# Performance work log

Hardware: AMD Instinct MI355X
Metric: run time of the kernel (lower is better)

The kernel has to match this reference:

```python
import jax, jax.numpy as jnp
import numpy as np

ALPHA = 0.2  # LeakyReLU negative slope
EPS = 1e-8


def setup_inputs() -> dict:
    key = jax.random.key(0)
    ks = jax.random.split(key, 7)
    N, Fin, Fout, E = 100000, 256, 128, 800000
    node_embedding = jax.random.normal(ks[0], (N, Fin), dtype=jnp.float32)
    adj_pos = jax.random.randint(ks[1], (2, E), 0, N, dtype=jnp.int64)
    adj_neg = jax.random.randint(ks[2], (2, E), 0, N, dtype=jnp.int64)
    edge_embedding = jax.random.normal(ks[3], (2, Fout), dtype=jnp.float32)
    Wr = jax.random.normal(ks[4], (2, Fin, Fout), dtype=jnp.float32) * 0.05
    a = jax.random.normal(ks[5], (1, 2 * Fout), dtype=jnp.float32) * 0.05
    bias = jax.random.normal(ks[6], (1, Fout), dtype=jnp.float32) * 0.05
    return dict(node_embedding=node_embedding, edge_embedding=edge_embedding,
                Wr=Wr, a=a, bias=bias, adj_pos=adj_pos, adj_neg=adj_neg)


def reference(node_embedding, edge_embedding, Wr, a, bias, adj_pos, adj_neg):
    N = node_embedding.shape[0]
    Fout = Wr.shape[2]
    # h_r = X @ Wr[r], then column-scale by edge_embedding[r] (== mm with diag)
    h_pos = (node_embedding @ Wr[0]) * edge_embedding[0]  # [N, Fout]
    h_neg = (node_embedding @ Wr[1]) * edge_embedding[1]  # [N, Fout]
    a_src = a[0, :Fout]  # attention weights for source half of concat
    a_dst = a[0, Fout:]  # attention weights for dest half

    def edge_scores(h, adj):
        # a . [h[src], h[dst]] computed as node-level dots then scalar gather
        s = h @ a_src  # [N]
        d = h @ a_dst  # [N]
        z = s[adj[0]] + d[adj[1]]  # [E]
        z = jnp.where(z > 0, z, ALPHA * z)  # LeakyReLU
        return jax.nn.sigmoid(z)

    e_pos = edge_scores(h_pos, adj_pos)  # [E_pos]
    e_neg = edge_scores(h_neg, adj_neg)  # [E_neg]

    # row-sum normalizer: spmm(edge, edge_e, ones) == segment_sum over row idx
    rows = jnp.concatenate([adj_pos[0], adj_neg[0]])
    e_all = jnp.concatenate([e_pos, e_neg])
    row_sum = jax.ops.segment_sum(e_all, rows, num_segments=N) + EPS  # [N]

    # weighted aggregation: out[i] = sum_{(i,j)} e_ij * h[j]
    agg = (jax.ops.segment_sum(e_pos[:, None] * h_pos[adj_pos[1]], adj_pos[0], num_segments=N)
           + jax.ops.segment_sum(e_neg[:, None] * h_neg[adj_neg[1]], adj_neg[0], num_segments=N))
    return agg / row_sum[:, None] + bias
```

## Files before the change

kernel.cpp:

```cpp
#include <hip/hip_runtime.h>

#define ALPHA 0.2f
#define EPSV 1e-8f
#define BUCK_BITS 8
#define BUCK (1 << BUCK_BITS)
#define CAP 5120
#define EPB_A 4096
#define EPT_A (EPB_A / 256)

typedef float f32x4 __attribute__((ext_vector_type(4)));
typedef short bf16x8 __attribute__((ext_vector_type(8)));

static __device__ __forceinline__ unsigned short f2bf(float f) {
    union { float f; unsigned int u; } c; c.f = f;
    unsigned int u = c.u;
    unsigned int round = ((u >> 16) & 1) + 0x7FFF;
    return (unsigned short)((u + round) >> 16);
}
static __device__ __forceinline__ float bflo(unsigned int u) {
    union { unsigned int u; float f; } c; c.u = u << 16; return c.f;
}
static __device__ __forceinline__ float bfhi(unsigned int u) {
    union { unsigned int u; float f; } c; c.u = u & 0xFFFF0000u; return c.f;
}

__global__ __launch_bounds__(256) void convB_binA_kernel(
    const float* __restrict__ Wr, uint4* __restrict__ Bp,
    const int* __restrict__ adj_pos, const int* __restrict__ adj_neg,
    int* __restrict__ bucketCount, unsigned int* __restrict__ edges_tmp,
    int N, int E)
{
    __shared__ int hist[512];
    __shared__ int base[512];
    __shared__ int cur[512];
    const int tid = threadIdx.x;

    if ((int)blockIdx.x < 32) {
        const int t = blockIdx.x * 256 + tid;
        const int kb  = t >> 8;
        const int col = t & 255;
        const int rel = col >> 7;
        const int cc  = col & 127;
        unsigned short v[8];
        #pragma unroll
        for (int jj = 0; jj < 8; ++jj) {
            const int k = kb * 8 + jj;
            v[jj] = f2bf(Wr[(size_t)rel * 256 * 128 + (size_t)k * 128 + cc]);
        }
        Bp[t] = *reinterpret_cast<const uint4*>(v);
        return;
    }

    const int bb = blockIdx.x - 32;
    const long long e0 = (long long)bb * EPB_A;
    const long long twoE = 2LL * E;

    hist[tid] = 0;
    hist[tid + 256] = 0;

    int esrc[EPT_A];
    unsigned int erec[EPT_A];
    #pragma unroll
    for (int k = 0; k < EPT_A; ++k) {
        const long long idx = e0 + (long long)k * 256 + tid;
        if (idx < twoE) {
            const int rel = (idx >= E) ? 1 : 0;
            const long long eidx = rel ? idx - E : idx;
            const int* __restrict__ adj = rel ? adj_neg : adj_pos;
            const int src = adj[eidx];
            const int dst = adj[E + eidx];
            esrc[k] = src;
            erec[k] = (unsigned int)dst | ((unsigned int)rel << 17) |
                      ((unsigned int)(src & (BUCK - 1)) << 18);
        } else {
            esrc[k] = -1;
        }
    }
    __syncthreads();

    #pragma unroll
    for (int k = 0; k < EPT_A; ++k)
        if (esrc[k] >= 0) atomicAdd(&hist[esrc[k] >> BUCK_BITS], 1);
    __syncthreads();

    {
        const int rot = (bb * 61) & 511;
        #pragma unroll
        for (int q = 0; q < 2; ++q) {
            const int t2 = (tid + q * 256 + rot) & 511;
            const int hv = hist[t2];
            base[t2] = hv ? atomicAdd(&bucketCount[t2], hv) : 0;
            cur[t2] = 0;
        }
    }
    __syncthreads();

    #pragma unroll
    for (int k = 0; k < EPT_A; ++k) {
        if (esrc[k] >= 0) {
            const int b = esrc[k] >> BUCK_BITS;
            const int r = atomicAdd(&cur[b], 1);
            const int pos = base[b] + r;
            if (pos < CAP)
                edges_tmp[(size_t)b * CAP + pos] = erec[k];
        }
    }
}

__global__ __launch_bounds__(256) void mfma_gemm_kernel(
    const float* __restrict__ X, const uint4* __restrict__ Bp,
    const float* __restrict__ ee, const float* __restrict__ a,
    unsigned short* __restrict__ h, float* __restrict__ sd, int N)
{
    __shared__ unsigned short Alds[32 * 256];
    const int tid  = threadIdx.x;
    const int lane = tid & 63;
    const int w    = tid >> 6;
    const int wm   = w >> 1;
    const int wn   = w & 1;
    const int cl   = lane & 15;
    const int g    = lane >> 4;
    const int tile0 = blockIdx.x * 32;

    #pragma unroll
    for (int pass = 0; pass < 4; ++pass) {
        const int L  = pass * 256 + tid;
        const int r  = L >> 5;
        const int c8 = L & 31;
        const int row = tile0 + r;
        float4 f0 = make_float4(0.f, 0.f, 0.f, 0.f);
        float4 f1 = make_float4(0.f, 0.f, 0.f, 0.f);
        if (row < N) {
            const float* xp = &X[(size_t)row * 256 + c8 * 8];
            f0 = *reinterpret_cast<const float4*>(xp);
            f1 = *reinterpret_cast<const float4*>(xp + 4);
        }
        unsigned short v[8];
        v[0]=f2bf(f0.x); v[1]=f2bf(f0.y); v[2]=f2bf(f0.z); v[3]=f2bf(f0.w);
        v[4]=f2bf(f1.x); v[5]=f2bf(f1.y); v[6]=f2bf(f1.z); v[7]=f2bf(f1.w);
        const int su = c8 ^ (r & 7);
        *reinterpret_cast<bf16x8*>(&Alds[r * 256 + su * 8]) =
            *reinterpret_cast<const bf16x8*>(v);
    }
    __syncthreads();

    f32x4 acc[8];
    #pragma unroll
    for (int ct = 0; ct < 8; ++ct)
        acc[ct] = (f32x4){0.f, 0.f, 0.f, 0.f};

    const int rl = wm * 16 + cl;
    #pragma unroll
    for (int kc = 0; kc < 8; ++kc) {
        const int ku = kc * 4 + g;
        const int su = ku ^ (rl & 7);
        const bf16x8 af = *reinterpret_cast<const bf16x8*>(&Alds[rl * 256 + su * 8]);
        bf16x8 bfr[8];
        #pragma unroll
        for (int ct = 0; ct < 8; ++ct) {
            const int col = wn * 128 + ct * 16 + cl;
            bfr[ct] = *reinterpret_cast<const bf16x8*>(Bp + ku * 256 + col);
        }
        #pragma unroll
        for (int ct = 0; ct < 8; ++ct)
            acc[ct] = __builtin_amdgcn_mfma_f32_16x16x32_bf16(
                af, bfr[ct], acc[ct], 0, 0, 0);
    }

    const int rt = blockIdx.x * 2 + wm;
    float eev[8], asv[8], adv[8];
    #pragma unroll
    for (int ct = 0; ct < 8; ++ct) {
        const int col = wn * 128 + ct * 16 + cl;
        const int cc  = col & 127;
        eev[ct] = ee[col];
        asv[ct] = a[cc];
        adv[ct] = a[128 + cc];
    }

    float s_acc[4], d_acc[4];
    #pragma unroll
    for (int reg = 0; reg < 4; ++reg) {
        const int row = rt * 16 + g * 4 + reg;
        const bool ok = row < N;
        float sp = 0.f, dp = 0.f;
        #pragma unroll
        for (int ct = 0; ct < 8; ++ct) {
            const float v = acc[ct][reg] * eev[ct];
            sp += v * asv[ct];
            dp += v * adv[ct];
            if (ok) {
                const int cc = ct * 16 + cl;
                h[((size_t)wn * N + row) * 128 + cc] = f2bf(v);
            }
        }
        s_acc[reg] = sp;
        d_acc[reg] = dp;
    }
    #pragma unroll
    for (int reg = 0; reg < 4; ++reg) {
        float sp = s_acc[reg], dp = d_acc[reg];
        #pragma unroll
        for (int off = 1; off < 16; off <<= 1) {
            sp += __shfl_xor(sp, off);
            dp += __shfl_xor(dp, off);
        }
        if (cl == 0) {
            const int row = rt * 16 + g * 4 + reg;
            if (row < N) {
                sd[(size_t)wn * 2 * N + row]     = sp;
                sd[(size_t)wn * 2 * N + N + row] = dp;
            }
        }
    }
}

__global__ __launch_bounds__(512) void sortB_kernel(
    const int* __restrict__ bucketCount, const unsigned int* __restrict__ edges_tmp,
    const float* __restrict__ sd,
    uint2* __restrict__ edges_final,
    int* __restrict__ rowBeg, int* __restrict__ rowEnd,
    float* __restrict__ rowSum, int N)
{
    __shared__ int hist[BUCK];
    __shared__ int cur[BUCK];
    __shared__ int ssum[BUCK];
    __shared__ float sSrc[2][BUCK];
    __shared__ float rsLds[BUCK];
    const int tid = threadIdx.x;
    const int b   = blockIdx.x;
    const int s0  = b << BUCK_BITS;
    const size_t tb = (size_t)b * CAP;
    const int cnt = min(bucketCount[b], CAP);

    if (tid < BUCK) {
        hist[tid] = 0;
        rsLds[tid] = 0.f;
        const int gsrc = s0 + tid;
        sSrc[0][tid] = (gsrc < N) ? sd[gsrc] : 0.f;
        sSrc[1][tid] = (gsrc < N) ? sd[2 * (size_t)N + gsrc] : 0.f;
    }
    __syncthreads();
    for (int j = tid; j < cnt; j += 512)
        atomicAdd(&hist[edges_tmp[tb + j] >> 18], 1);
    __syncthreads();

    int h0 = 0, incl = 0;
    if (tid < BUCK) { h0 = hist[tid]; ssum[tid] = h0; incl = h0; }
    __syncthreads();
    for (int off = 1; off < BUCK; off <<= 1) {
        const int u = (tid < BUCK && tid >= off) ? ssum[tid - off] : 0;
        __syncthreads();
        if (tid < BUCK) { incl += u; ssum[tid] = incl; }
        __syncthreads();
    }
    if (tid < BUCK) {
        const int excl = incl - h0;
        cur[tid] = excl;
        const int gidx = s0 + tid;
        if (gidx < N) {
            rowBeg[gidx] = (int)tb + excl;
            rowEnd[gidx] = (int)tb + incl;
        }
    }
    __syncthreads();
    for (int j = tid; j < cnt; j += 512) {
        const unsigned int r = edges_tmp[tb + j];
        const int sl  = r >> 18;
        const int rel = (r >> 17) & 1;
        const int dst = r & 0x1FFFF;
        float z = sSrc[rel][sl] + sd[(size_t)rel * 2 * N + N + dst];
        z = z > 0.f ? z : ALPHA * z;
        const float ev = 1.f / (1.f + __expf(-z));
        const int pos = atomicAdd(&cur[sl], 1);
        atomicAdd(&rsLds[sl], ev);
        edges_final[tb + pos] =
            make_uint2((unsigned int)(rel * N + dst), __float_as_uint(ev));
    }
    __syncthreads();
    if (tid < BUCK) {
        const int gidx = s0 + tid;
        if (gidx < N) rowSum[gidx] = rsLds[tid];
    }
}

__global__ __launch_bounds__(256) void gather_kernel(
    const int* __restrict__ rowBeg, const int* __restrict__ rowEnd,
    const float* __restrict__ rowSum,
    const uint2* __restrict__ edges,
    const unsigned short* __restrict__ h,
    const float* __restrict__ bias, float* __restrict__ out, int N)
{
    const long long gw = ((long long)blockIdx.x * blockDim.x + threadIdx.x) >> 6;
    const int lane = threadIdx.x & 63;
    if (gw >= N) return;
    const int n = (int)gw;

    const int beg = rowBeg[n];
    const int end = rowEnd[n];
    const unsigned loff = (unsigned)(lane << 2);
    const char* __restrict__ hb = (const char*)h;

    float ax = 0.f, ay = 0.f;
    int j = beg;
    for (; j + 8 <= end; j += 8) {
        uint2 r[8];
        #pragma unroll
        for (int k = 0; k < 8; ++k) r[k] = edges[j + k];
        unsigned int hv[8];
        #pragma unroll
        for (int k = 0; k < 8; ++k)
            hv[k] = *reinterpret_cast<const unsigned int*>(
                hb + ((r[k].x << 8) + loff));
        #pragma unroll
        for (int k = 0; k < 8; ++k) {
            const float e = __uint_as_float(r[k].y);
            ax += e * bflo(hv[k]);
            ay += e * bfhi(hv[k]);
        }
    }
    for (; j + 4 <= end; j += 4) {
        uint2 r[4];
        #pragma unroll
        for (int k = 0; k < 4; ++k) r[k] = edges[j + k];
        unsigned int hv[4];
        #pragma unroll
        for (int k = 0; k < 4; ++k)
            hv[k] = *reinterpret_cast<const unsigned int*>(
                hb + ((r[k].x << 8) + loff));
        #pragma unroll
        for (int k = 0; k < 4; ++k) {
            const float e = __uint_as_float(r[k].y);
            ax += e * bflo(hv[k]);
            ay += e * bfhi(hv[k]);
        }
    }
    for (; j < end; ++j) {
        const uint2 r = edges[j];
        const unsigned int hv = *reinterpret_cast<const unsigned int*>(
            hb + ((r.x << 8) + loff));
        const float e = __uint_as_float(r.y);
        ax += e * bflo(hv);
        ay += e * bfhi(hv);
    }
    const float inv = 1.f / (rowSum[n] + EPSV);
    const float2 bv = *reinterpret_cast<const float2*>(&bias[lane * 2]);
    float2 o;
    o.x = ax * inv + bv.x;
    o.y = ay * inv + bv.y;
    *reinterpret_cast<float2*>(&out[(size_t)n * 128 + lane * 2]) = o;
}

extern "C" void kernel_launch(void* const* d_in, const int* in_sizes, int n_in,
                              void* d_out, int out_size, void* d_ws, size_t ws_size,
                              hipStream_t stream) {
    const float* X      = (const float*)d_in[0];
    const float* ee     = (const float*)d_in[1];
    const float* Wr     = (const float*)d_in[2];
    const float* a      = (const float*)d_in[3];
    const float* bias   = (const float*)d_in[4];
    const int* adj_pos  = (const int*)d_in[5];
    const int* adj_neg  = (const int*)d_in[6];

    const int N = in_sizes[0] / 256;
    const int E = in_sizes[5] / 2;
    const int twoE = 2 * E;
    float* out = (float*)d_out;

    const int gemmBlocks = (N + 31) / 32;
    const int NBUCK = (N + BUCK - 1) >> BUCK_BITS;
    const int binBlocks = (twoE + EPB_A - 1) / EPB_A;

    char* ws = (char*)d_ws;
    uint4* Bp = (uint4*)ws;
    char* p = ws + 32 * 256 * 16;
    unsigned short* h = (unsigned short*)p; p += (size_t)2 * N * 128 * 2;
    float* sd         = (float*)p;  p += (size_t)4 * N * 4;
    int* bucketCount  = (int*)p;    p += 512 * 4;
    int* rowBeg       = (int*)p;    p += (size_t)N * 4;
    int* rowEnd       = (int*)p;    p += (size_t)N * 4;
    float* rowSum     = (float*)p;  p += (size_t)N * 4;
    p = (char*)(((uintptr_t)p + 15) & ~(uintptr_t)15);
    unsigned int* edges_tmp = (unsigned int*)p; p += (size_t)NBUCK * CAP * 4;
    uint2* edges_final = (uint2*)p; p += (size_t)NBUCK * CAP * 8;

    (void)hipMemsetAsync(bucketCount, 0, 512 * sizeof(int), stream);

    convB_binA_kernel<<<32 + binBlocks, 256, 0, stream>>>(
        Wr, Bp, adj_pos, adj_neg, bucketCount, edges_tmp, N, E);

    mfma_gemm_kernel<<<gemmBlocks, 256, 0, stream>>>(X, Bp, ee, a, h, sd, N);

    sortB_kernel<<<NBUCK, 512, 0, stream>>>(
        bucketCount, edges_tmp, sd, edges_final, rowBeg, rowEnd, rowSum, N);

    gather_kernel<<<(int)(((long long)N * 64 + 255) / 256), 256, 0, stream>>>(
        rowBeg, rowEnd, rowSum, edges_final, (const unsigned short*)h, bias, out, N);
}
```

Measured before the change: 169.7 us.

## Pack h as bf16 pairs, prefetch GEMM operands, batch X loads

The GEMM epilogue now packs two bf16 outputs into one 32-bit store using a permuted column layout, replacing eight 2-byte scattered stores per row. The gather kernel un-permutes the columns when writing the output. The GEMM also issues all X global loads before converting any of them, and double-buffers the B/A fragments across k-steps to overlap loads with MFMA. These changes raise register pressure, and the gather output stores become scalar rather than float2.

```diff
diff --git a/kernel.cpp b/kernel.cpp
--- a/kernel.cpp
+++ b/kernel.cpp
@@ -110,7 +110,7 @@
 __global__ __launch_bounds__(256) void mfma_gemm_kernel(
     const float* __restrict__ X, const uint4* __restrict__ Bp,
     const float* __restrict__ ee, const float* __restrict__ a,
-    unsigned short* __restrict__ h, float* __restrict__ sd, int N)
+    unsigned int* __restrict__ h32, float* __restrict__ sd, int N)
 {
     __shared__ unsigned short Alds[32 * 256];
     const int tid  = threadIdx.x;
@@ -122,25 +122,36 @@
     const int g    = lane >> 4;
     const int tile0 = blockIdx.x * 32;
 
-    #pragma unroll
-    for (int pass = 0; pass < 4; ++pass) {
-        const int L  = pass * 256 + tid;
-        const int r  = L >> 5;
-        const int c8 = L & 31;
-        const int row = tile0 + r;
-        float4 f0 = make_float4(0.f, 0.f, 0.f, 0.f);
-        float4 f1 = make_float4(0.f, 0.f, 0.f, 0.f);
-        if (row < N) {
-            const float* xp = &X[(size_t)row * 256 + c8 * 8];
-            f0 = *reinterpret_cast<const float4*>(xp);
-            f1 = *reinterpret_cast<const float4*>(xp + 4);
-        }
-        unsigned short v[8];
-        v[0]=f2bf(f0.x); v[1]=f2bf(f0.y); v[2]=f2bf(f0.z); v[3]=f2bf(f0.w);
-        v[4]=f2bf(f1.x); v[5]=f2bf(f1.y); v[6]=f2bf(f1.z); v[7]=f2bf(f1.w);
-        const int su = c8 ^ (r & 7);
-        *reinterpret_cast<bf16x8*>(&Alds[r * 256 + su * 8]) =
-            *reinterpret_cast<const bf16x8*>(v);
+    {
+        float4 fa[4], fb[4];
+        #pragma unroll
+        for (int pass = 0; pass < 4; ++pass) {
+            const int L  = pass * 256 + tid;
+            const int r  = L >> 5;
+            const int c8 = L & 31;
+            const int row = tile0 + r;
+            fa[pass] = make_float4(0.f, 0.f, 0.f, 0.f);
+            fb[pass] = make_float4(0.f, 0.f, 0.f, 0.f);
+            if (row < N) {
+                const float* xp = &X[(size_t)row * 256 + c8 * 8];
+                fa[pass] = *reinterpret_cast<const float4*>(xp);
+                fb[pass] = *reinterpret_cast<const float4*>(xp + 4);
+            }
+        }
+        #pragma unroll
+        for (int pass = 0; pass < 4; ++pass) {
+            const int L  = pass * 256 + tid;
+            const int r  = L >> 5;
+            const int c8 = L & 31;
+            unsigned short v[8];
+            v[0]=f2bf(fa[pass].x); v[1]=f2bf(fa[pass].y);
+            v[2]=f2bf(fa[pass].z); v[3]=f2bf(fa[pass].w);
+            v[4]=f2bf(fb[pass].x); v[5]=f2bf(fb[pass].y);
+            v[6]=f2bf(fb[pass].z); v[7]=f2bf(fb[pass].w);
+            const int su = c8 ^ (r & 7);
+            *reinterpret_cast<bf16x8*>(&Alds[r * 256 + su * 8]) =
+                *reinterpret_cast<const bf16x8*>(v);
+        }
     }
     __syncthreads();
 
@@ -150,21 +161,39 @@
         acc[ct] = (f32x4){0.f, 0.f, 0.f, 0.f};
 
     const int rl = wm * 16 + cl;
-    #pragma unroll
-    for (int kc = 0; kc < 8; ++kc) {
-        const int ku = kc * 4 + g;
-        const int su = ku ^ (rl & 7);
-        const bf16x8 af = *reinterpret_cast<const bf16x8*>(&Alds[rl * 256 + su * 8]);
-        bf16x8 bfr[8];
+    bf16x8 bcur[8], acur;
+    {
+        const int ku = g;
         #pragma unroll
         for (int ct = 0; ct < 8; ++ct) {
             const int col = wn * 128 + ct * 16 + cl;
-            bfr[ct] = *reinterpret_cast<const bf16x8*>(Bp + ku * 256 + col);
+            bcur[ct] = *reinterpret_cast<const bf16x8*>(Bp + ku * 256 + col);
+        }
+        acur = *reinterpret_cast<const bf16x8*>(
+            &Alds[rl * 256 + (ku ^ (rl & 7)) * 8]);
+    }
+    #pragma unroll
+    for (int kc = 0; kc < 8; ++kc) {
+        bf16x8 bnext[8], anext;
+        if (kc < 7) {
+            const int ku = (kc + 1) * 4 + g;
+            #pragma unroll
+            for (int ct = 0; ct < 8; ++ct) {
+                const int col = wn * 128 + ct * 16 + cl;
+                bnext[ct] = *reinterpret_cast<const bf16x8*>(Bp + ku * 256 + col);
+            }
+            anext = *reinterpret_cast<const bf16x8*>(
+                &Alds[rl * 256 + (ku ^ (rl & 7)) * 8]);
         }
         #pragma unroll
         for (int ct = 0; ct < 8; ++ct)
             acc[ct] = __builtin_amdgcn_mfma_f32_16x16x32_bf16(
-                af, bfr[ct], acc[ct], 0, 0, 0);
+                acur, bcur[ct], acc[ct], 0, 0, 0);
+        if (kc < 7) {
+            #pragma unroll
+            for (int ct = 0; ct < 8; ++ct) bcur[ct] = bnext[ct];
+            acur = anext;
+        }
     }
 
     const int rt = blockIdx.x * 2 + wm;
@@ -184,14 +213,20 @@
         const int row = rt * 16 + g * 4 + reg;
         const bool ok = row < N;
         float sp = 0.f, dp = 0.f;
+        float vv[8];
         #pragma unroll
         for (int ct = 0; ct < 8; ++ct) {
-            const float v = acc[ct][reg] * eev[ct];
-            sp += v * asv[ct];
-            dp += v * adv[ct];
-            if (ok) {
-                const int cc = ct * 16 + cl;
-                h[((size_t)wn * N + row) * 128 + cc] = f2bf(v);
+            vv[ct] = acc[ct][reg] * eev[ct];
+            sp += vv[ct] * asv[ct];
+            dp += vv[ct] * adv[ct];
+        }
+        if (ok) {
+            #pragma unroll
+            for (int q = 0; q < 4; ++q) {
+                const unsigned int u =
+                    (unsigned int)f2bf(vv[2 * q]) |
+                    ((unsigned int)f2bf(vv[2 * q + 1]) << 16);
+                h32[((size_t)wn * N + row) * 64 + q * 16 + cl] = u;
             }
         }
         s_acc[reg] = sp;
@@ -288,7 +323,7 @@
     const int* __restrict__ rowBeg, const int* __restrict__ rowEnd,
     const float* __restrict__ rowSum,
     const uint2* __restrict__ edges,
-    const unsigned short* __restrict__ h,
+    const unsigned int* __restrict__ h32,
     const float* __restrict__ bias, float* __restrict__ out, int N)
 {
     const long long gw = ((long long)blockIdx.x * blockDim.x + threadIdx.x) >> 6;
@@ -299,7 +334,7 @@
     const int beg = rowBeg[n];
     const int end = rowEnd[n];
     const unsigned loff = (unsigned)(lane << 2);
-    const char* __restrict__ hb = (const char*)h;
+    const char* __restrict__ hb = (const char*)h32;
 
     float ax = 0.f, ay = 0.f;
     int j = beg;
@@ -344,11 +379,12 @@
         ay += e * bfhi(hv);
     }
     const float inv = 1.f / (rowSum[n] + EPSV);
-    const float2 bv = *reinterpret_cast<const float2*>(&bias[lane * 2]);
-    float2 o;
-    o.x = ax * inv + bv.x;
-    o.y = ay * inv + bv.y;
-    *reinterpret_cast<float2*>(&out[(size_t)n * 128 + lane * 2]) = o;
+    const int q  = lane >> 4;
+    const int cl = lane & 15;
+    const int c0 = q * 32 + cl;
+    const int c1 = c0 + 16;
+    out[(size_t)n * 128 + c0] = ax * inv + bias[c0];
+    out[(size_t)n * 128 + c1] = ay * inv + bias[c1];
 }
 
 extern "C" void kernel_launch(void* const* d_in, const int* in_sizes, int n_in,
@@ -374,7 +410,7 @@
     char* ws = (char*)d_ws;
     uint4* Bp = (uint4*)ws;
     char* p = ws + 32 * 256 * 16;
-    unsigned short* h = (unsigned short*)p; p += (size_t)2 * N * 128 * 2;
+    unsigned int* h32 = (unsigned int*)p; p += (size_t)2 * N * 64 * 4;
     float* sd         = (float*)p;  p += (size_t)4 * N * 4;
     int* bucketCount  = (int*)p;    p += 512 * 4;
     int* rowBeg       = (int*)p;    p += (size_t)N * 4;
@@ -389,11 +425,11 @@
     convB_binA_kernel<<<32 + binBlocks, 256, 0, stream>>>(
         Wr, Bp, adj_pos, adj_neg, bucketCount, edges_tmp, N, E);
 
-    mfma_gemm_kernel<<<gemmBlocks, 256, 0, stream>>>(X, Bp, ee, a, h, sd, N);
+    mfma_gemm_kernel<<<gemmBlocks, 256, 0, stream>>>(X, Bp, ee, a, h32, sd, N);
 
     sortB_kernel<<<NBUCK, 512, 0, stream>>>(
         bucketCount, edges_tmp, sd, edges_final, rowBeg, rowEnd, rowSum, N);
 
     gather_kernel<<<(int)(((long long)N * 64 + 255) / 256), 256, 0, stream>>>(
-        rowBeg, rowEnd, rowSum, edges_final, (const unsigned short*)h, bias, out, N);
-}
+        rowBeg, rowEnd, rowSum, edges_final, h32, bias, out, N);
+}
```

After: 171.4 us. Within noise of the previous version (+1.0%).
